# Performance work log

Measured on AMD Instinct MI355X. Metric: run time of the kernel, lower is better.

Reference implementation:

```python
import jax, jax.numpy as jnp
import numpy as np

BETA = 0.25

def setup_inputs() -> dict:
    key = jax.random.key(0)
    k1, k2 = jax.random.split(key)
    z = jax.random.normal(k1, (32, 64, 64, 64), dtype=jnp.float32)  # (B, D, H, W)
    # EmbeddingEMA init: uniform(-1/K, 1/K)
    K, D = 1024, 64
    weight = jax.random.uniform(k2, (K, D), dtype=jnp.float32, minval=-1.0 / K, maxval=1.0 / K)
    return {"z": z, "weight": weight}


def reference(z, weight):
    b, d, h, w = z.shape
    K = weight.shape[0]
    # permute (B,D,H,W) -> (B,H,W,D) and flatten to (N, D)
    z_flat = jnp.transpose(z, (0, 2, 3, 1)).reshape(-1, d)
    # squared euclidean distance: ||z||^2 + ||c||^2 - 2 z c^T  -> (N, K)
    distance = (
        jnp.sum(z_flat * z_flat, axis=1, keepdims=True)
        + jnp.sum(weight * weight, axis=1)
        - 2.0 * jnp.matmul(z_flat, weight.T)
    )
    vq_indices = jnp.argmin(distance, axis=1)  # (N,)
    z_quantized = weight[vq_indices]  # gather (N, D)
    # one-hot scatter stats (training-time EMA inputs)
    vq_current_count = jax.ops.segment_sum(
        jnp.ones((z_flat.shape[0],), dtype=z_flat.dtype), vq_indices, num_segments=K)
    vq_current_sum = jax.ops.segment_sum(z_flat, vq_indices, num_segments=K)  # (K, D)
    commitment_loss = jnp.mean((z_flat - jax.lax.stop_gradient(z_quantized)) ** 2)
    loss = BETA * commitment_loss
    # straight-through estimator
    q = z_flat + jax.lax.stop_gradient(z_quantized - z_flat)
    q = jnp.transpose(q.reshape(b, h, w, d), (0, 3, 1, 2))  # back to (B, D, H, W)
    return q, loss, commitment_loss, vq_current_count, vq_current_sum
```

## Files before the change

### kernel.cpp

```cpp
#include <hip/hip_runtime.h>


#define HWsz   4096
#define Dd     64
#define Kk     1024
#define NB     32
#define NTOT   131072
#define QSIZE  (NTOT * Dd)
#define BETA_C 0.25f
#define DIST_BLOCKS 1024
#define NCHUNK 16

typedef float  f32x4  __attribute__((ext_vector_type(4)));
typedef short  bf16x8 __attribute__((ext_vector_type(8)));

__device__ __forceinline__ unsigned short f2bf(float f) {
    unsigned u = __float_as_uint(f);
    u += 0x7FFF + ((u >> 16) & 1);
    return (unsigned short)(u >> 16);
}
__device__ __forceinline__ float bf2f(unsigned short b) {
    return __uint_as_float(((unsigned)b) << 16);
}

__device__ __forceinline__ void stage16(const void* g, void* lds, int lane) {
#if __has_builtin(__builtin_amdgcn_global_load_lds)
    __builtin_amdgcn_global_load_lds(
        (const __attribute__((address_space(1))) unsigned int*)g,
        (__attribute__((address_space(3))) unsigned int*)lds, 16, 0, 0);
#else
    *(bf16x8*)((unsigned short*)lds + lane * 8) = *(const bf16x8*)g;
#endif
}

__global__ __launch_bounds__(256) void vq_prep(const float* __restrict__ w,
                                               float* __restrict__ c2,
                                               unsigned short* __restrict__ whi,
                                               unsigned short* __restrict__ wlo) {
    int t = blockIdx.x * 256 + threadIdx.x;
    int k = t >> 6, d = t & 63;
    float v = w[t];
    unsigned short hb = f2bf(v);
    unsigned short lb = f2bf(v - bf2f(hb));
    int ctile = k >> 4, col = k & 15;
    int s = d >> 5, kg = (d >> 3) & 3, j = d & 7;
    int idx = (((ctile * 2 + s) * 64) + kg * 16 + col) * 8 + j;
    whi[idx] = hb; wlo[idx] = lb;

    if (t < Kk) {
        const float4* c4 = reinterpret_cast<const float4*>(w + t * Dd);
        float s0 = 0.f, s1 = 0.f, s2 = 0.f, s3 = 0.f;
#pragma unroll
        for (int q = 0; q < 16; ++q) {
            float4 cq = c4[q];
            s0 = fmaf(cq.x, cq.x, s0); s1 = fmaf(cq.y, cq.y, s1);
            s2 = fmaf(cq.z, cq.z, s2); s3 = fmaf(cq.w, cq.w, s3);
        }
        c2[t] = (s0 + s1) + (s2 + s3);
    }
}

__global__ __launch_bounds__(128, 3) void vq_dist(const float* __restrict__ z,
                                                  const float* __restrict__ w,
                                                  const float* __restrict__ c2,
                                                  const unsigned short* __restrict__ whi,
                                                  const unsigned short* __restrict__ wlo,
                                                  float* __restrict__ out,
                                                  float* __restrict__ commit_ws,
                                                  int* __restrict__ idx_ws) {
    const int lane = threadIdx.x & 63;
    const int wid  = threadIdx.x >> 6;
    const int b    = blockIdx.x >> 5;
    const int hwb  = (blockIdx.x & 31) * 128 + wid * 64;
    const int col  = lane & 15;
    const int kg   = lane >> 4;

    __shared__ unsigned short lbuf[2][8192];

    bf16x8 zhi[4][2], zlo[4][2];
#pragma unroll
    for (int m = 0; m < 4; ++m) {
        const float* zbase = z + (size_t)b * (Dd * HWsz) + (hwb + m * 16) + col;
#pragma unroll
        for (int s = 0; s < 2; ++s) {
            bf16x8 h, l;
#pragma unroll
            for (int j = 0; j < 8; ++j) {
                float zz = zbase[(size_t)(32 * s + kg * 8 + j) * HWsz];
                unsigned short hb = f2bf(zz);
                unsigned short lb = f2bf(zz - bf2f(hb));
                h[j] = (short)hb; l[j] = (short)lb;
            }
            zhi[m][s] = h; zlo[m][s] = l;
        }
    }

    const char* ghi = (const char*)whi;
    const char* glo = (const char*)wlo;
#define STAGE(c, bufi)                                                          \
    {                                                                           \
        unsigned short* dst = lbuf[bufi];                                       \
        _Pragma("unroll")                                                       \
        for (int rd = 0; rd < 4; ++rd) {                                        \
            int rec = ((c) * 8 + rd * 2 + wid) * 1024 + lane * 16;              \
            stage16(ghi + rec, dst + rd * 2048 + wid * 512, lane);              \
            stage16(glo + rec, dst + rd * 2048 + (2 + wid) * 512, lane);        \
        }                                                                       \
    }

    float best[4][4];
    int   bk[4][4];
#pragma unroll
    for (int m = 0; m < 4; ++m)
#pragma unroll
        for (int r = 0; r < 4; ++r) { best[m][r] = 3.4e38f; bk[m][r] = 0; }

    STAGE(0, 0);
    __syncthreads();

    for (int c = 0; c < NCHUNK; ++c) {
        const unsigned short* cb = lbuf[c & 1];
        if (c + 1 < NCHUNK) STAGE(c + 1, (c + 1) & 1);
#pragma unroll
        for (int t = 0; t < 4; ++t) {
            const int ct = c * 4 + t;
            bf16x8 wh0 = *(const bf16x8*)(cb + t * 2048 + 0 * 512 + lane * 8);
            bf16x8 wh1 = *(const bf16x8*)(cb + t * 2048 + 1 * 512 + lane * 8);
            bf16x8 wl0 = *(const bf16x8*)(cb + t * 2048 + 2 * 512 + lane * 8);
            bf16x8 wl1 = *(const bf16x8*)(cb + t * 2048 + 3 * 512 + lane * 8);
            const float cv = c2[ct * 16 + col];
            const int   kc = ct * 16 + col;

            f32x4 za[4];
#pragma unroll
            for (int m = 0; m < 4; ++m) za[m] = (f32x4){0.f, 0.f, 0.f, 0.f};
#pragma unroll
            for (int m = 0; m < 4; ++m)
                za[m] = __builtin_amdgcn_mfma_f32_16x16x32_bf16(zhi[m][0], wh0, za[m], 0, 0, 0);
#pragma unroll
            for (int m = 0; m < 4; ++m)
                za[m] = __builtin_amdgcn_mfma_f32_16x16x32_bf16(zhi[m][1], wh1, za[m], 0, 0, 0);
#pragma unroll
            for (int m = 0; m < 4; ++m)
                za[m] = __builtin_amdgcn_mfma_f32_16x16x32_bf16(zhi[m][0], wl0, za[m], 0, 0, 0);
#pragma unroll
            for (int m = 0; m < 4; ++m)
                za[m] = __builtin_amdgcn_mfma_f32_16x16x32_bf16(zhi[m][1], wl1, za[m], 0, 0, 0);
#pragma unroll
            for (int m = 0; m < 4; ++m)
                za[m] = __builtin_amdgcn_mfma_f32_16x16x32_bf16(zlo[m][0], wh0, za[m], 0, 0, 0);
#pragma unroll
            for (int m = 0; m < 4; ++m)
                za[m] = __builtin_amdgcn_mfma_f32_16x16x32_bf16(zlo[m][1], wh1, za[m], 0, 0, 0);

#pragma unroll
            for (int m = 0; m < 4; ++m)
#pragma unroll
                for (int r = 0; r < 4; ++r) {
                    float s = fmaf(-2.f, za[m][r], cv);
                    if (s < best[m][r]) { best[m][r] = s; bk[m][r] = kc; }
                }
        }
        __syncthreads();
    }

#pragma unroll
    for (int off = 1; off < 16; off <<= 1) {
#pragma unroll
        for (int m = 0; m < 4; ++m)
#pragma unroll
            for (int r = 0; r < 4; ++r) {
                float ob = __shfl_xor(best[m][r], off, 64);
                int   ok = __shfl_xor(bk[m][r],   off, 64);
                if (ob < best[m][r] || (ob == best[m][r] && ok < bk[m][r])) {
                    best[m][r] = ob; bk[m][r] = ok;
                }
            }
    }

    float commit = 0.f;
    const int srcl = (col >> 2) << 4;
    const int rsel = col & 3;
#pragma unroll
    for (int m = 0; m < 4; ++m) {
        int c0 = __shfl(bk[m][0], srcl, 64);
        int c1 = __shfl(bk[m][1], srcl, 64);
        int c2r = __shfl(bk[m][2], srcl, 64);
        int c3 = __shfl(bk[m][3], srcl, 64);
        int mybk = (rsel == 0) ? c0 : (rsel == 1) ? c1 : (rsel == 2) ? c2r : c3;

        const int hw0 = hwb + m * 16;
        if (lane < 16) idx_ws[(size_t)b * HWsz + hw0 + col] = mybk;

        float* qbase = out + (size_t)b * (Dd * HWsz) + hw0 + col;
#pragma unroll
        for (int s = 0; s < 2; ++s) {
            const float4* cw = reinterpret_cast<const float4*>(w + mybk * Dd + 32 * s + kg * 8);
            float4 p0 = cw[0], p1 = cw[1];
            float cbv[8] = {p0.x, p0.y, p0.z, p0.w, p1.x, p1.y, p1.z, p1.w};
#pragma unroll
            for (int j = 0; j < 8; ++j) {
                int   d  = 32 * s + kg * 8 + j;
                float zz = bf2f((unsigned short)zhi[m][s][j]) +
                           bf2f((unsigned short)zlo[m][s][j]);
                float cc = cbv[j];
                qbase[(size_t)d * HWsz] = zz + (cc - zz);
                float dd = zz - cc;
                commit = fmaf(dd, dd, commit);
            }
        }
    }

#pragma unroll
    for (int off = 32; off > 0; off >>= 1) commit += __shfl_down(commit, off, 64);

    __shared__ float red[2];
    if (lane == 0) red[wid] = commit;
    __syncthreads();
    if (threadIdx.x == 0) commit_ws[blockIdx.x] = red[0] + red[1];
}

__global__ __launch_bounds__(256) void vq_stats(const float* __restrict__ z,
                                                const int* __restrict__ idx_ws,
                                                float* __restrict__ psum,
                                                float* __restrict__ pcnt) {
    const int b  = blockIdx.x >> 5;
    const int dp = blockIdx.x & 31;
    const int d0 = dp * 2;
    const bool docnt = (dp == 0);

    __shared__ float acc0[Kk], acc1[Kk], cnt[Kk];
    for (int i = threadIdx.x; i < Kk; i += 256) { acc0[i] = 0.f; acc1[i] = 0.f; cnt[i] = 0.f; }
    __syncthreads();

    const int4*   ip  = reinterpret_cast<const int4*>(idx_ws + (size_t)b * HWsz);
    const float4* zp0 = reinterpret_cast<const float4*>(z + ((size_t)b * Dd + d0) * HWsz);
    const float4* zp1 = reinterpret_cast<const float4*>(z + ((size_t)b * Dd + d0 + 1) * HWsz);
#pragma unroll
    for (int it = 0; it < 4; ++it) {
        int c4 = it * 256 + threadIdx.x;
        int4   k4 = ip[c4];
        float4 v0 = zp0[c4];
        float4 v1 = zp1[c4];
        atomicAdd(&acc0[k4.x], v0.x); atomicAdd(&acc0[k4.y], v0.y);
        atomicAdd(&acc0[k4.z], v0.z); atomicAdd(&acc0[k4.w], v0.w);
        atomicAdd(&acc1[k4.x], v1.x); atomicAdd(&acc1[k4.y], v1.y);
        atomicAdd(&acc1[k4.z], v1.z); atomicAdd(&acc1[k4.w], v1.w);
        if (docnt) {
            atomicAdd(&cnt[k4.x], 1.f); atomicAdd(&cnt[k4.y], 1.f);
            atomicAdd(&cnt[k4.z], 1.f); atomicAdd(&cnt[k4.w], 1.f);
        }
    }
    __syncthreads();

    float* po = psum + ((size_t)b * Dd + d0) * Kk;
    for (int i = threadIdx.x; i < Kk; i += 256) { po[i] = acc0[i]; po[Kk + i] = acc1[i]; }
    if (docnt) {
        float* pc = pcnt + (size_t)b * Kk;
        for (int i = threadIdx.x; i < Kk; i += 256) pc[i] = cnt[i];
    }
}

__global__ __launch_bounds__(256) void vq_reduce(const float* __restrict__ psum,
                                                 const float* __restrict__ pcnt,
                                                 const float* __restrict__ commit_ws,
                                                 float* __restrict__ out) {
    int t = blockIdx.x * 256 + threadIdx.x;
    int k = t & 1023, d = t >> 10;
    float s = 0.f;
#pragma unroll
    for (int b = 0; b < NB; ++b)
        s += psum[((size_t)b * Dd + d) * Kk + k];
    out[QSIZE + 2 + Kk + (size_t)k * Dd + d] = s;
    if (t < Kk) {
        float c = 0.f;
#pragma unroll
        for (int b = 0; b < NB; ++b) c += pcnt[((size_t)b << 10) + t];
        out[QSIZE + 2 + t] = c;
    }

    if (blockIdx.x == 0) {
        float cs = 0.f;
        for (int i = threadIdx.x; i < DIST_BLOCKS; i += 256) cs += commit_ws[i];
#pragma unroll
        for (int off = 32; off > 0; off >>= 1) cs += __shfl_down(cs, off, 64);
        __shared__ float r2[4];
        const int lane = threadIdx.x & 63, wid = threadIdx.x >> 6;
        if (lane == 0) r2[wid] = cs;
        __syncthreads();
        if (threadIdx.x == 0) {
            float c = ((r2[0] + r2[1]) + (r2[2] + r2[3])) / (float)QSIZE;
            out[QSIZE]     = BETA_C * c;
            out[QSIZE + 1] = c;
        }
    }
}

extern "C" void kernel_launch(void* const* d_in, const int* in_sizes, int n_in,
                              void* d_out, int out_size, void* d_ws, size_t ws_size,
                              hipStream_t stream) {
    const float* z = (const float*)d_in[0];
    const float* w = (const float*)d_in[1];
    float* out = (float*)d_out;

    float* commit_ws = (float*)d_ws;
    float* c2        = (float*)d_ws + 1024;
    unsigned short* whi = (unsigned short*)((float*)d_ws + 2048);
    unsigned short* wlo = whi + (Kk * Dd);
    int*   idx_ws = (int*)(wlo + (Kk * Dd));
    float* pcnt   = (float*)(idx_ws + NTOT);
    float* psum   = pcnt + (size_t)NB * Kk;

    vq_prep<<<(Kk * Dd) / 256, 256, 0, stream>>>(w, c2, whi, wlo);
    vq_dist<<<DIST_BLOCKS, 128, 0, stream>>>(z, w, c2, whi, wlo, out, commit_ws, idx_ws);
    vq_stats<<<NB * 32, 256, 0, stream>>>(z, idx_ws, psum, pcnt);
    vq_reduce<<<(Kk * Dd) / 256, 256, 0, stream>>>(psum, pcnt, commit_ws, out);
}
```

Baseline: 236.1 us.

## Switch distance kernel to 32x32 MFMA with direct register codebook loads

Rewrites the distance kernel to use 32x32x16 bf16 MFMA tiles, with each wave owning 32 rows instead of 64 and blocks of 256 threads. The LDS double-buffer staging and per-chunk barriers are dropped. Codebook hi/lo fragments are now loaded straight from global memory (L2-resident) into registers with a two-way software prefetch. The codebook prep layout is changed to match the new fragment shape. This cuts LDS traffic and synchronisation but puts more cache load on every wave and keeps fewer rows per wave to reuse each codebook fragment.

```diff
diff --git a/kernel.cpp b/kernel.cpp
--- a/kernel.cpp
+++ b/kernel.cpp
@@ -9,10 +9,11 @@
 #define QSIZE  (NTOT * Dd)
 #define BETA_C 0.25f
 #define DIST_BLOCKS 1024
-#define NCHUNK 16
-
-typedef float  f32x4  __attribute__((ext_vector_type(4)));
+
+typedef float  f32x16 __attribute__((ext_vector_type(16)));
 typedef short  bf16x8 __attribute__((ext_vector_type(8)));
+
+#define MF32(a, b, c) __builtin_amdgcn_mfma_f32_32x32x16_bf16((a), (b), (c), 0, 0, 0)
 
 __device__ __forceinline__ unsigned short f2bf(float f) {
     unsigned u = __float_as_uint(f);
@@ -21,16 +22,6 @@
 }
 __device__ __forceinline__ float bf2f(unsigned short b) {
     return __uint_as_float(((unsigned)b) << 16);
-}
-
-__device__ __forceinline__ void stage16(const void* g, void* lds, int lane) {
-#if __has_builtin(__builtin_amdgcn_global_load_lds)
-    __builtin_amdgcn_global_load_lds(
-        (const __attribute__((address_space(1))) unsigned int*)g,
-        (__attribute__((address_space(3))) unsigned int*)lds, 16, 0, 0);
-#else
-    *(bf16x8*)((unsigned short*)lds + lane * 8) = *(const bf16x8*)g;
-#endif
 }
 
 __global__ __launch_bounds__(256) void vq_prep(const float* __restrict__ w,
@@ -42,9 +33,10 @@
     float v = w[t];
     unsigned short hb = f2bf(v);
     unsigned short lb = f2bf(v - bf2f(hb));
-    int ctile = k >> 4, col = k & 15;
-    int s = d >> 5, kg = (d >> 3) & 3, j = d & 7;
-    int idx = (((ctile * 2 + s) * 64) + kg * 16 + col) * 8 + j;
+    int ct = k >> 5, col = k & 31;
+    int s = d >> 4, half = (d >> 3) & 1, j = d & 7;
+    int lane = half * 32 + col;
+    int idx = (((ct * 4 + s) * 64) + lane) * 8 + j;
     whi[idx] = hb; wlo[idx] = lb;
 
     if (t < Kk) {
@@ -60,164 +52,140 @@
     }
 }
 
-__global__ __launch_bounds__(128, 3) void vq_dist(const float* __restrict__ z,
-                                                  const float* __restrict__ w,
-                                                  const float* __restrict__ c2,
-                                                  const unsigned short* __restrict__ whi,
-                                                  const unsigned short* __restrict__ wlo,
-                                                  float* __restrict__ out,
-                                                  float* __restrict__ commit_ws,
-                                                  int* __restrict__ idx_ws) {
+__global__ __launch_bounds__(256) void vq_dist(const float* __restrict__ z,
+                                               const float* __restrict__ w,
+                                               const float* __restrict__ c2,
+                                               const unsigned short* __restrict__ whi,
+                                               const unsigned short* __restrict__ wlo,
+                                               float* __restrict__ out,
+                                               float* __restrict__ commit_ws,
+                                               int* __restrict__ idx_ws) {
     const int lane = threadIdx.x & 63;
     const int wid  = threadIdx.x >> 6;
     const int b    = blockIdx.x >> 5;
-    const int hwb  = (blockIdx.x & 31) * 128 + wid * 64;
-    const int col  = lane & 15;
-    const int kg   = lane >> 4;
-
-    __shared__ unsigned short lbuf[2][8192];
-
-    bf16x8 zhi[4][2], zlo[4][2];
-#pragma unroll
-    for (int m = 0; m < 4; ++m) {
-        const float* zbase = z + (size_t)b * (Dd * HWsz) + (hwb + m * 16) + col;
-#pragma unroll
-        for (int s = 0; s < 2; ++s) {
-            bf16x8 h, l;
-#pragma unroll
-            for (int j = 0; j < 8; ++j) {
-                float zz = zbase[(size_t)(32 * s + kg * 8 + j) * HWsz];
-                unsigned short hb = f2bf(zz);
-                unsigned short lb = f2bf(zz - bf2f(hb));
-                h[j] = (short)hb; l[j] = (short)lb;
+    const int hwb  = (blockIdx.x & 31) * 128 + wid * 32;
+    const int c32  = lane & 31;
+    const int dh   = (lane >> 5) * 8;
+
+    const float* zbase = z + (size_t)b * (Dd * HWsz) + hwb + c32;
+    bf16x8 zhi[4], zlo[4];
+#pragma unroll
+    for (int s = 0; s < 4; ++s) {
+        bf16x8 h, l;
+#pragma unroll
+        for (int j = 0; j < 8; ++j) {
+            float zz = zbase[(size_t)(16 * s + dh + j) * HWsz];
+            unsigned short hb = f2bf(zz);
+            unsigned short lb = f2bf(zz - bf2f(hb));
+            h[j] = (short)hb; l[j] = (short)lb;
+        }
+        zhi[s] = h; zlo[s] = l;
+    }
+
+    float best[16];
+    int   bk[16];
+#pragma unroll
+    for (int r = 0; r < 16; ++r) { best[r] = 3.4e38f; bk[r] = 0; }
+
+    const bf16x8* pha = reinterpret_cast<const bf16x8*>(whi) + lane;
+    const bf16x8* pla = reinterpret_cast<const bf16x8*>(wlo) + lane;
+    const bf16x8* phb = pha + 256;
+    const bf16x8* plb = pla + 256;
+    const float*  cvp = c2 + c32;
+
+#define LOADB(H0, H1, H2, H3, L0, L1, L2, L3, CV, PH, PL, CTI)   \
+    {                                                            \
+        H0 = (PH)[0 * 64]; H1 = (PH)[1 * 64];                    \
+        H2 = (PH)[2 * 64]; H3 = (PH)[3 * 64];                    \
+        L0 = (PL)[0 * 64]; L1 = (PL)[1 * 64];                    \
+        L2 = (PL)[2 * 64]; L3 = (PL)[3 * 64];                    \
+        CV = cvp[(CTI) * 32];                                    \
+    }
+
+#define COMPUTE(H0, H1, H2, H3, L0, L1, L2, L3, CV, CT)                        \
+    {                                                                          \
+        f32x16 p = {0.f,0.f,0.f,0.f,0.f,0.f,0.f,0.f,0.f,0.f,0.f,0.f,0.f,0.f,0.f,0.f}; \
+        f32x16 q = {0.f,0.f,0.f,0.f,0.f,0.f,0.f,0.f,0.f,0.f,0.f,0.f,0.f,0.f,0.f,0.f}; \
+        p = MF32(zhi[0], H0, p);  q = MF32(zhi[2], H2, q);                     \
+        p = MF32(zhi[1], H1, p);  q = MF32(zhi[3], H3, q);                     \
+        p = MF32(zlo[0], H0, p);  q = MF32(zlo[2], H2, q);                     \
+        p = MF32(zlo[1], H1, p);  q = MF32(zlo[3], H3, q);                     \
+        p = MF32(zhi[0], L0, p);  q = MF32(zhi[2], L2, q);                     \
+        p = MF32(zhi[1], L1, p);  q = MF32(zhi[3], L3, q);                     \
+        const int kc = (CT) * 32 + c32;                                        \
+        _Pragma("unroll")                                                      \
+        for (int r = 0; r < 16; ++r) {                                         \
+            float sc = fmaf(-2.f, p[r] + q[r], CV);                            \
+            if (sc < best[r]) { best[r] = sc; bk[r] = kc; }                    \
+        }                                                                      \
+    }
+
+    bf16x8 aH0, aH1, aH2, aH3, aL0, aL1, aL2, aL3;
+    bf16x8 bH0, bH1, bH2, bH3, bL0, bL1, bL2, bL3;
+    float  acv, bcv;
+
+    LOADB(aH0, aH1, aH2, aH3, aL0, aL1, aL2, aL3, acv, pha, pla, 0);
+
+    for (int it = 0; it < 16; ++it) {
+        const int ct = it * 2;
+        LOADB(bH0, bH1, bH2, bH3, bL0, bL1, bL2, bL3, bcv, phb, plb, ct + 1);
+        COMPUTE(aH0, aH1, aH2, aH3, aL0, aL1, aL2, aL3, acv, ct);
+        pha += 512; pla += 512;
+        if (it < 15)
+            LOADB(aH0, aH1, aH2, aH3, aL0, aL1, aL2, aL3, acv, pha, pla, ct + 2);
+        COMPUTE(bH0, bH1, bH2, bH3, bL0, bL1, bL2, bL3, bcv, ct + 1);
+        phb += 512; plb += 512;
+    }
+
+#pragma unroll
+    for (int off = 1; off < 32; off <<= 1) {
+#pragma unroll
+        for (int r = 0; r < 16; ++r) {
+            float ob = __shfl_xor(best[r], off, 64);
+            int   ok = __shfl_xor(bk[r],   off, 64);
+            if (ob < best[r] || (ob == best[r] && ok < bk[r])) {
+                best[r] = ob; bk[r] = ok;
             }
-            zhi[m][s] = h; zlo[m][s] = l;
-        }
-    }
-
-    const char* ghi = (const char*)whi;
-    const char* glo = (const char*)wlo;
-#define STAGE(c, bufi)                                                          \
-    {                                                                           \
-        unsigned short* dst = lbuf[bufi];                                       \
-        _Pragma("unroll")                                                       \
-        for (int rd = 0; rd < 4; ++rd) {                                        \
-            int rec = ((c) * 8 + rd * 2 + wid) * 1024 + lane * 16;              \
-            stage16(ghi + rec, dst + rd * 2048 + wid * 512, lane);              \
-            stage16(glo + rec, dst + rd * 2048 + (2 + wid) * 512, lane);        \
-        }                                                                       \
-    }
-
-    float best[4][4];
-    int   bk[4][4];
-#pragma unroll
-    for (int m = 0; m < 4; ++m)
-#pragma unroll
-        for (int r = 0; r < 4; ++r) { best[m][r] = 3.4e38f; bk[m][r] = 0; }
-
-    STAGE(0, 0);
-    __syncthreads();
-
-    for (int c = 0; c < NCHUNK; ++c) {
-        const unsigned short* cb = lbuf[c & 1];
-        if (c + 1 < NCHUNK) STAGE(c + 1, (c + 1) & 1);
-#pragma unroll
-        for (int t = 0; t < 4; ++t) {
-            const int ct = c * 4 + t;
-            bf16x8 wh0 = *(const bf16x8*)(cb + t * 2048 + 0 * 512 + lane * 8);
-            bf16x8 wh1 = *(const bf16x8*)(cb + t * 2048 + 1 * 512 + lane * 8);
-            bf16x8 wl0 = *(const bf16x8*)(cb + t * 2048 + 2 * 512 + lane * 8);
-            bf16x8 wl1 = *(const bf16x8*)(cb + t * 2048 + 3 * 512 + lane * 8);
-            const float cv = c2[ct * 16 + col];
-            const int   kc = ct * 16 + col;
-
-            f32x4 za[4];
-#pragma unroll
-            for (int m = 0; m < 4; ++m) za[m] = (f32x4){0.f, 0.f, 0.f, 0.f};
-#pragma unroll
-            for (int m = 0; m < 4; ++m)
-                za[m] = __builtin_amdgcn_mfma_f32_16x16x32_bf16(zhi[m][0], wh0, za[m], 0, 0, 0);
-#pragma unroll
-            for (int m = 0; m < 4; ++m)
-                za[m] = __builtin_amdgcn_mfma_f32_16x16x32_bf16(zhi[m][1], wh1, za[m], 0, 0, 0);
-#pragma unroll
-            for (int m = 0; m < 4; ++m)
-                za[m] = __builtin_amdgcn_mfma_f32_16x16x32_bf16(zhi[m][0], wl0, za[m], 0, 0, 0);
-#pragma unroll
-            for (int m = 0; m < 4; ++m)
-                za[m] = __builtin_amdgcn_mfma_f32_16x16x32_bf16(zhi[m][1], wl1, za[m], 0, 0, 0);
-#pragma unroll
-            for (int m = 0; m < 4; ++m)
-                za[m] = __builtin_amdgcn_mfma_f32_16x16x32_bf16(zlo[m][0], wh0, za[m], 0, 0, 0);
-#pragma unroll
-            for (int m = 0; m < 4; ++m)
-                za[m] = __builtin_amdgcn_mfma_f32_16x16x32_bf16(zlo[m][1], wh1, za[m], 0, 0, 0);
-
-#pragma unroll
-            for (int m = 0; m < 4; ++m)
-#pragma unroll
-                for (int r = 0; r < 4; ++r) {
-                    float s = fmaf(-2.f, za[m][r], cv);
-                    if (s < best[m][r]) { best[m][r] = s; bk[m][r] = kc; }
-                }
-        }
-        __syncthreads();
-    }
-
-#pragma unroll
-    for (int off = 1; off < 16; off <<= 1) {
-#pragma unroll
-        for (int m = 0; m < 4; ++m)
-#pragma unroll
-            for (int r = 0; r < 4; ++r) {
-                float ob = __shfl_xor(best[m][r], off, 64);
-                int   ok = __shfl_xor(bk[m][r],   off, 64);
-                if (ob < best[m][r] || (ob == best[m][r] && ok < bk[m][r])) {
-                    best[m][r] = ob; bk[m][r] = ok;
-                }
-            }
-    }
-
+        }
+    }
+
+    const int hi5   = ((lane >> 2) & 1) << 5;
+    const int myreg = (lane & 3) + (((lane >> 3) & 3) << 2);
+    int mybk = 0;
+#pragma unroll
+    for (int re = 0; re < 16; ++re) {
+        int t = __shfl(bk[re], hi5, 64);
+        if (re == myreg) mybk = t;
+    }
+
+    if (lane < 32) idx_ws[(size_t)b * HWsz + hwb + lane] = mybk;
+
+    float* qbase = out + (size_t)b * (Dd * HWsz) + hwb + c32;
     float commit = 0.f;
-    const int srcl = (col >> 2) << 4;
-    const int rsel = col & 3;
-#pragma unroll
-    for (int m = 0; m < 4; ++m) {
-        int c0 = __shfl(bk[m][0], srcl, 64);
-        int c1 = __shfl(bk[m][1], srcl, 64);
-        int c2r = __shfl(bk[m][2], srcl, 64);
-        int c3 = __shfl(bk[m][3], srcl, 64);
-        int mybk = (rsel == 0) ? c0 : (rsel == 1) ? c1 : (rsel == 2) ? c2r : c3;
-
-        const int hw0 = hwb + m * 16;
-        if (lane < 16) idx_ws[(size_t)b * HWsz + hw0 + col] = mybk;
-
-        float* qbase = out + (size_t)b * (Dd * HWsz) + hw0 + col;
-#pragma unroll
-        for (int s = 0; s < 2; ++s) {
-            const float4* cw = reinterpret_cast<const float4*>(w + mybk * Dd + 32 * s + kg * 8);
-            float4 p0 = cw[0], p1 = cw[1];
-            float cbv[8] = {p0.x, p0.y, p0.z, p0.w, p1.x, p1.y, p1.z, p1.w};
-#pragma unroll
-            for (int j = 0; j < 8; ++j) {
-                int   d  = 32 * s + kg * 8 + j;
-                float zz = bf2f((unsigned short)zhi[m][s][j]) +
-                           bf2f((unsigned short)zlo[m][s][j]);
-                float cc = cbv[j];
-                qbase[(size_t)d * HWsz] = zz + (cc - zz);
-                float dd = zz - cc;
-                commit = fmaf(dd, dd, commit);
-            }
+#pragma unroll
+    for (int s = 0; s < 4; ++s) {
+        const float4* cw = reinterpret_cast<const float4*>(w + mybk * Dd + 16 * s + dh);
+        float4 p0 = cw[0], p1 = cw[1];
+        float cbv[8] = {p0.x, p0.y, p0.z, p0.w, p1.x, p1.y, p1.z, p1.w};
+#pragma unroll
+        for (int j = 0; j < 8; ++j) {
+            int   d  = 16 * s + dh + j;
+            float zz = bf2f((unsigned short)zhi[s][j]) + bf2f((unsigned short)zlo[s][j]);
+            float cc = cbv[j];
+            qbase[(size_t)d * HWsz] = zz + (cc - zz);
+            float dd = zz - cc;
+            commit = fmaf(dd, dd, commit);
         }
     }
 
 #pragma unroll
     for (int off = 32; off > 0; off >>= 1) commit += __shfl_down(commit, off, 64);
 
-    __shared__ float red[2];
+    __shared__ float red[4];
     if (lane == 0) red[wid] = commit;
     __syncthreads();
-    if (threadIdx.x == 0) commit_ws[blockIdx.x] = red[0] + red[1];
+    if (threadIdx.x == 0)
+        commit_ws[blockIdx.x] = (red[0] + red[1]) + (red[2] + red[3]);
 }
 
 __global__ __launch_bounds__(256) void vq_stats(const float* __restrict__ z,
@@ -312,7 +280,7 @@
     float* psum   = pcnt + (size_t)NB * Kk;
 
     vq_prep<<<(Kk * Dd) / 256, 256, 0, stream>>>(w, c2, whi, wlo);
-    vq_dist<<<DIST_BLOCKS, 128, 0, stream>>>(z, w, c2, whi, wlo, out, commit_ws, idx_ws);
+    vq_dist<<<DIST_BLOCKS, 256, 0, stream>>>(z, w, c2, whi, wlo, out, commit_ws, idx_ws);
     vq_stats<<<NB * 32, 256, 0, stream>>>(z, idx_ws, psum, pcnt);
     vq_reduce<<<(Kk * Dd) / 256, 256, 0, stream>>>(psum, pcnt, commit_ws, out);
 }
```

After: 243.9 us. 1.03x slower.
